# Optimization experiments

Hardware: AMD Instinct MI355X
Metric: run time of the kernel (lower is better)

Reference implementation:

```python
import jax, jax.numpy as jnp
import numpy as np
import math

D_MODEL = 2048
K = 64
W = 512              # window_size
STRIDE = W // 2      # = 256
EMA_ALPHA = 0.9
N_RETRIEVE = 8
EPS = 1e-12


def _build_cheby(k, w):
    # cheby_mat[k, n] = cos(k * arccos(t_n)), t_n = cos(pi*(2n+1)/(2w))
    ns = np.arange(w, dtype=np.float64)
    t = np.cos(np.pi * (2 * ns + 1) / (2 * w))
    ks = np.arange(k, dtype=np.float64)
    return jnp.asarray(np.cos(ks[:, None] * np.arccos(t)[None, :]), dtype=jnp.float32)


def setup_inputs() -> dict:
    key = jax.random.key(0)
    ks = jax.random.split(key, 5)
    B, S = 2, 8192
    scan_out = jax.random.normal(ks[0], (B, S, D_MODEL), dtype=jnp.float32)
    buf = jax.random.normal(ks[1], (W, D_MODEL), dtype=jnp.float32)  # pre-filled circular buffer
    # unit-modulus random-phase complex roles: r_k[d] = exp(i*theta)
    phases = jax.random.uniform(ks[2], (K, D_MODEL), dtype=jnp.float32) * (2.0 * math.pi)
    roles_real = jnp.cos(phases)
    roles_imag = jnp.sin(phases)
    w_bands = 1.0 / (jnp.arange(K, dtype=jnp.float32) + 1.0)  # w_init = 1/(k+1)
    retrieve_proj_w = jax.random.normal(ks[3], (D_MODEL, D_MODEL), dtype=jnp.float32) * 0.02
    inject_gate = jnp.zeros((1,), dtype=jnp.float32)
    cheby_mat = _build_cheby(K, W)
    return dict(scan_out=scan_out, buf=buf, roles_real=roles_real, roles_imag=roles_imag,
                w_bands=w_bands, retrieve_proj_w=retrieve_proj_w, inject_gate=inject_gate,
                cheby_mat=cheby_mat)


def reference(scan_out, buf, roles_real, roles_imag, w_bands, retrieve_proj_w, inject_gate, cheby_mat):
    S = scan_out.shape[1]
    h_mean = scan_out.mean(axis=0)                      # [S, D] batch-mean like torch code
    n_chunks = S // STRIDE
    chunks = h_mean.reshape(n_chunks, STRIDE, D_MODEL)  # each chunk triggers one bind

    init = (buf, jnp.int32(0),
            jnp.zeros((K, D_MODEL), jnp.float32),   # c_past
            jnp.zeros((D_MODEL,), jnp.float32),     # V_mem_real
            jnp.zeros((D_MODEL,), jnp.float32),     # V_mem_imag
            jnp.zeros((K,), jnp.float32),           # _coeff_norms (EMA)
            jnp.zeros((K,), jnp.float32))           # spectral_delta

    def step(carry, chunk):
        b, pos, c_past, vr, vi, cnorms, _ = carry
        # circular-buffer write of `stride` tokens starting at pos
        b = jax.lax.dynamic_update_slice(b, chunk, (pos, 0))
        pos = (pos + STRIDE) % W
        order = (jnp.arange(W, dtype=jnp.int32) + pos) % W   # oldest-first reorder
        data = b[order]                                      # [W, D]
        # Chebyshev coefficients: c = (2/W) * cheby_mat @ data, c0 halved
        coeffs = (2.0 / W) * (cheby_mat @ data)              # [K, D]
        coeffs = coeffs.at[0].multiply(0.5)
        # HRR-normalized bind into holographic memory via EMA
        norms = jnp.maximum(jnp.linalg.norm(coeffs, axis=-1, keepdims=True), EPS)
        cn = coeffs / norms
        cnorms = EMA_ALPHA * cnorms + (1.0 - EMA_ALPHA) * norms[:, 0]
        vr = EMA_ALPHA * vr + (1.0 - EMA_ALPHA) * (cn * roles_real).sum(axis=0)
        vi = EMA_ALPHA * vi + (1.0 - EMA_ALPHA) * (cn * roles_imag).sum(axis=0)
        # spectral delta vs previous window's coefficients
        delta = jnp.linalg.norm(coeffs - c_past, axis=-1)    # [K]
        return (b, pos, coeffs, vr, vi, cnorms, delta), None

    (b, pos, c_now, vr, vi, cnorms, delta), _ = jax.lax.scan(step, init, chunks)

    # retrieve: unbind top-J bands by spectral delta, denormalize, weight, project
    _, top = jax.lax.top_k(delta, N_RETRIEVE)                # [J]
    rr = roles_real[top]
    ri = roles_imag[top]
    retrieved = (vr[None, :] * rr + vi[None, :] * ri) * jnp.maximum(cnorms[top], EPS)[:, None]  # [J, D]
    weights = jax.nn.softplus(w_bands[top])                  # [J]
    ctx = (weights[:, None] * retrieved).sum(axis=0)         # [D]
    out = (ctx @ retrieve_proj_w.T) * jax.nn.sigmoid(inject_gate[0])  # [D]
    return out, delta, vr, vi
```

## Files before the change

### kernel.cpp

```cpp
#include <hip/hip_runtime.h>
#include <math.h>

#define D_MODEL 2048
#define KB_ 64
#define NCHUNK 32

typedef __bf16 bf16;
typedef __attribute__((ext_vector_type(8))) __bf16 bf16x8;
typedef __attribute__((ext_vector_type(4))) __bf16 bf16x4;
typedef __attribute__((ext_vector_type(4))) float f32x4;

#define OFF_PQ 0
#define N_PQ (33 * 128 * 2048)
#define OFF_NORMS N_PQ
#define OFF_PARTR (OFF_NORMS + 2048)
#define OFF_PARTI (OFF_PARTR + 32 * 2048)
#define OFF_CTX (OFF_PARTI + 32 * 2048)

__global__ __launch_bounds__(256, 4) void k1_mfma(
    const float* __restrict__ scan, const float* __restrict__ buf,
    const float* __restrict__ cheby, float* __restrict__ PQ)
{
  __shared__ bf16 As[128 * 72];
  __shared__ bf16 Bs[128 * 72];

  const int t = threadIdx.x;
  const int dtile = blockIdx.x, j = blockIdx.y;
  const int wid = t >> 6, lane = t & 63;
  const int wm = wid >> 1, wn = wid & 1;
  const int quad = lane >> 4, r16 = lane & 15;
  const int d0 = dtile * 128;
  const float* scan1 = scan + 8192 * 2048;

  f32x4 acc[4][4];
#pragma unroll
  for (int a = 0; a < 4; ++a)
#pragma unroll
    for (int b = 0; b < 4; ++b) acc[a][b] = (f32x4){0.f, 0.f, 0.f, 0.f};

  for (int nb = 0; nb < 4; ++nb) {
    __syncthreads();
#pragma unroll
    for (int i = 0; i < 8; ++i) {
      int flat = t + i * 256;
      int b = flat >> 4, q4 = flat & 15;
      const float* src = (b < 64) ? (cheby + b * 512 + nb * 64)
                                  : (cheby + (b - 64) * 512 + 256 + nb * 64);
      float4 v = *(const float4*)(src + q4 * 4);
      bf16x4 e = {(bf16)v.x, (bf16)v.y, (bf16)v.z, (bf16)v.w};
      *(bf16x4*)(As + b * 72 + q4 * 4) = e;
    }
#pragma unroll
    for (int i = 0; i < 8; ++i) {
      int p = t + i * 256;
      int d = p & 127;
      int n0 = (p >> 7) * 4;
      float v[4];
      if (j == 0) {
#pragma unroll
        for (int x = 0; x < 4; ++x)
          v[x] = buf[(256 + nb * 64 + n0 + x) * 2048 + d0 + d];
      } else {
        int base = ((j - 1) * 256 + nb * 64 + n0) * 2048 + d0 + d;
#pragma unroll
        for (int x = 0; x < 4; ++x)
          v[x] = 0.5f * (scan[base + x * 2048] + scan1[base + x * 2048]);
      }
      bf16x4 e = {(bf16)v[0], (bf16)v[1], (bf16)v[2], (bf16)v[3]};
      *(bf16x4*)(Bs + d * 72 + n0) = e;
    }
    __syncthreads();

#pragma unroll
    for (int ks = 0; ks < 2; ++ks) {
      bf16x8 af[4], bfr[4];
#pragma unroll
      for (int tm = 0; tm < 4; ++tm)
        af[tm] = *(const bf16x8*)(As + (wm * 64 + tm * 16 + r16) * 72 + ks * 32 + quad * 8);
#pragma unroll
      for (int tn = 0; tn < 4; ++tn)
        bfr[tn] = *(const bf16x8*)(Bs + (wn * 64 + tn * 16 + r16) * 72 + ks * 32 + quad * 8);
#pragma unroll
      for (int tm = 0; tm < 4; ++tm)
#pragma unroll
        for (int tn = 0; tn < 4; ++tn)
          acc[tm][tn] = __builtin_amdgcn_mfma_f32_16x16x32_bf16(
              af[tm], bfr[tn], acc[tm][tn], 0, 0, 0);
    }
  }

  const float scale = 2.0f / 512.0f;
#pragma unroll
  for (int tm = 0; tm < 4; ++tm) {
    int band_base = wm * 64 + tm * 16 + quad * 4;
#pragma unroll
    for (int tn = 0; tn < 4; ++tn) {
      int dc = d0 + wn * 64 + tn * 16 + r16;
#pragma unroll
      for (int r = 0; r < 4; ++r) {
        int band = band_base + r;
        float sc = (band == 0 || band == 64) ? scale * 0.5f : scale;
        PQ[(j * 128 + band) * 2048 + dc] = acc[tm][tn][r] * sc;
      }
    }
  }
}

__global__ __launch_bounds__(256) void k2_norms(
    const float* __restrict__ PQ, float* __restrict__ norms,
    float* __restrict__ dout)
{
  const int tid = threadIdx.x;
  const int b = blockIdx.x;
  float s = 0.f;
  if (b < NCHUNK * KB_) {
    int c = b >> 6, k = b & 63;
    const float* P = PQ + (c * 128 + k) * 2048;
    const float* Q = PQ + ((c + 1) * 128 + 64 + k) * 2048;
#pragma unroll
    for (int i = 0; i < 2; ++i) {
      float4 p = *(const float4*)(P + tid * 4 + i * 1024);
      float4 q = *(const float4*)(Q + tid * 4 + i * 1024);
      float x = p.x + q.x, y = p.y + q.y, z = p.z + q.z, w = p.w + q.w;
      s += x * x + y * y + z * z + w * w;
    }
  } else {
    int k = b - NCHUNK * KB_;
    const float* P1 = PQ + (31 * 128 + k) * 2048;
    const float* Q2 = PQ + (32 * 128 + 64 + k) * 2048;
    const float* P0 = PQ + (30 * 128 + k) * 2048;
    const float* Q1 = PQ + (31 * 128 + 64 + k) * 2048;
#pragma unroll
    for (int i = 0; i < 2; ++i) {
      float4 a = *(const float4*)(P1 + tid * 4 + i * 1024);
      float4 bb = *(const float4*)(Q2 + tid * 4 + i * 1024);
      float4 cc = *(const float4*)(P0 + tid * 4 + i * 1024);
      float4 dd = *(const float4*)(Q1 + tid * 4 + i * 1024);
      float x = a.x + bb.x - cc.x - dd.x, y = a.y + bb.y - cc.y - dd.y;
      float z = a.z + bb.z - cc.z - dd.z, w = a.w + bb.w - cc.w - dd.w;
      s += x * x + y * y + z * z + w * w;
    }
  }
  for (int o = 32; o > 0; o >>= 1) s += __shfl_down(s, o, 64);
  __shared__ float red[4];
  if ((tid & 63) == 0) red[tid >> 6] = s;
  __syncthreads();
  if (tid == 0) {
    float r = sqrtf(red[0] + red[1] + red[2] + red[3]);
    if (b < NCHUNK * KB_) norms[b] = fmaxf(r, 1e-12f);
    else dout[D_MODEL + (b - NCHUNK * KB_)] = r;
  }
}

__global__ __launch_bounds__(256) void k3_bind(
    const float* __restrict__ PQ, const float* __restrict__ norms,
    const float* __restrict__ rr, const float* __restrict__ ri,
    float* __restrict__ part_r, float* __restrict__ part_i)
{
  const int d4 = (blockIdx.x * 256 + threadIdx.x) * 4;
  const int c = blockIdx.y;
  const float wc = 0.1f * powf(0.9f, (float)(31 - c));
  float4 ar = make_float4(0.f, 0.f, 0.f, 0.f);
  float4 ai = make_float4(0.f, 0.f, 0.f, 0.f);
  for (int k = 0; k < KB_; ++k) {
    float4 p = *(const float4*)(PQ + (c * 128 + k) * 2048 + d4);
    float4 q = *(const float4*)(PQ + ((c + 1) * 128 + 64 + k) * 2048 + d4);
    float inv = 1.0f / norms[c * KB_ + k];
    float4 r = *(const float4*)(rr + k * D_MODEL + d4);
    float4 im = *(const float4*)(ri + k * D_MODEL + d4);
    float cx = (p.x + q.x) * inv, cy = (p.y + q.y) * inv;
    float cz = (p.z + q.z) * inv, cw = (p.w + q.w) * inv;
    ar.x += cx * r.x; ar.y += cy * r.y; ar.z += cz * r.z; ar.w += cw * r.w;
    ai.x += cx * im.x; ai.y += cy * im.y; ai.z += cz * im.z; ai.w += cw * im.w;
  }
  float4 outr = make_float4(wc * ar.x, wc * ar.y, wc * ar.z, wc * ar.w);
  float4 outi = make_float4(wc * ai.x, wc * ai.y, wc * ai.z, wc * ai.w);
  *(float4*)(part_r + c * D_MODEL + d4) = outr;
  *(float4*)(part_i + c * D_MODEL + d4) = outi;
}

__global__ __launch_bounds__(256) void k4_ctx(
    const float* __restrict__ norms, const float* __restrict__ part_r,
    const float* __restrict__ part_i, const float* __restrict__ rr,
    const float* __restrict__ ri, const float* __restrict__ wbands,
    float* __restrict__ dout, float* __restrict__ ctx)
{
  __shared__ float cn_s[64];
  __shared__ int top_s[8];
  __shared__ float wgt_s[8];
  const int tid = threadIdx.x;
  const int d = blockIdx.x * 256 + tid;
  if (tid < 64) {
    float s = 0.f;
    for (int c = 0; c < NCHUNK; ++c) s = 0.9f * s + 0.1f * norms[c * KB_ + tid];
    cn_s[tid] = fmaxf(s, 1e-12f);
  }
  __syncthreads();
  if (tid == 0) {
    unsigned long long taken = 0ULL;
    for (int jj = 0; jj < 8; ++jj) {
      float best = -1.f;
      int bi = 0;
      for (int k = 0; k < 64; ++k) {
        float dv = dout[D_MODEL + k];
        if (!((taken >> k) & 1ULL) && dv > best) { best = dv; bi = k; }
      }
      taken |= (1ULL << bi);
      top_s[jj] = bi;
      wgt_s[jj] = log1pf(expf(wbands[bi]));
    }
  }
  __syncthreads();
  float sr = 0.f, si = 0.f;
  for (int c = 0; c < NCHUNK; ++c) {
    sr += part_r[c * D_MODEL + d];
    si += part_i[c * D_MODEL + d];
  }
  dout[D_MODEL + KB_ + d] = sr;
  dout[D_MODEL + KB_ + D_MODEL + d] = si;
  float cx = 0.f;
#pragma unroll
  for (int jj = 0; jj < 8; ++jj) {
    int k = top_s[jj];
    cx += wgt_s[jj] * (sr * rr[k * D_MODEL + d] + si * ri[k * D_MODEL + d]) * cn_s[k];
  }
  ctx[d] = cx;
}

__global__ __launch_bounds__(256) void k5b_gemv(
    const float* __restrict__ Wp, const float* __restrict__ ctx,
    const float* __restrict__ gate, float* __restrict__ dout)
{
  const int tid = threadIdx.x;
  const int lane = tid & 63;
  const int w = tid >> 6;
  const int row = blockIdx.x * 4 + w;
  const float* p = Wp + row * D_MODEL;
  float s = 0.f;
#pragma unroll
  for (int i = 0; i < 8; ++i) {
    int e = lane * 4 + i * 256;
    float4 wv = *(const float4*)(p + e);
    float4 cv = *(const float4*)(ctx + e);
    s += wv.x * cv.x + wv.y * cv.y + wv.z * cv.z + wv.w * cv.w;
  }
  for (int o = 32; o > 0; o >>= 1) s += __shfl_down(s, o, 64);
  if (lane == 0) {
    float sig = 1.f / (1.f + expf(-gate[0]));
    dout[row] = s * sig;
  }
}

extern "C" void kernel_launch(void* const* d_in, const int* in_sizes, int n_in,
                              void* d_out, int out_size, void* d_ws, size_t ws_size,
                              hipStream_t stream) {
  const float* scan  = (const float*)d_in[0];
  const float* buf   = (const float*)d_in[1];
  const float* rr    = (const float*)d_in[2];
  const float* ri    = (const float*)d_in[3];
  const float* wb    = (const float*)d_in[4];
  const float* Wp    = (const float*)d_in[5];
  const float* gate  = (const float*)d_in[6];
  const float* cheby = (const float*)d_in[7];
  float* out = (float*)d_out;
  float* ws = (float*)d_ws;

  float* PQ     = ws + OFF_PQ;
  float* norms  = ws + OFF_NORMS;
  float* part_r = ws + OFF_PARTR;
  float* part_i = ws + OFF_PARTI;
  float* ctx    = ws + OFF_CTX;

  k1_mfma<<<dim3(16, 33), 256, 0, stream>>>(scan, buf, cheby, PQ);
  k2_norms<<<NCHUNK * KB_ + KB_, 256, 0, stream>>>(PQ, norms, out);
  k3_bind<<<dim3(2, NCHUNK), 256, 0, stream>>>(PQ, norms, rr, ri, part_r, part_i);
  k4_ctx<<<8, 256, 0, stream>>>(norms, part_r, part_i, rr, ri, wb, out, ctx);
  k5b_gemv<<<512, 256, 0, stream>>>(Wp, ctx, gate, out);
}
```

Baseline: 301.8 us.

## Compute full-window coefficients directly in MFMA kernel and fuse norm partials

Before, per-half-window partial coefficients (P/Q) were computed and summed in later kernels. Now each block handles one chunk's full 512-sample window against pre-converted bf16 Chebyshev rows and writes the final coefficients directly. The epilogue also emits per-tile squared-norm partials, which removes the separate norms kernel and the P+Q re-reads in the bind kernel. In exchange, overlapping scan rows are read twice, since adjacent windows share half their samples, and a small prep kernel and a delta kernel are added.

Result: faster. 279.6 us (-7.4%).

```diff
diff --git a/kernel.cpp b/kernel.cpp
--- a/kernel.cpp
+++ b/kernel.cpp
@@ -10,173 +10,165 @@
 typedef __attribute__((ext_vector_type(4))) __bf16 bf16x4;
 typedef __attribute__((ext_vector_type(4))) float f32x4;
 
-#define OFF_PQ 0
-#define N_PQ (33 * 128 * 2048)
-#define OFF_NORMS N_PQ
-#define OFF_PARTR (OFF_NORMS + 2048)
-#define OFF_PARTI (OFF_PARTR + 32 * 2048)
-#define OFF_CTX (OFF_PARTI + 32 * 2048)
-
-__global__ __launch_bounds__(256, 4) void k1_mfma(
+#define OFF_COEFFS 0
+#define OFF_NSQ    (32 * 64 * 2048)
+#define OFF_NORMS  (OFF_NSQ + 32 * 64 * 32)
+#define OFF_PARTR  (OFF_NORMS + 2048)
+#define OFF_PARTI  (OFF_PARTR + 32 * 2048)
+#define OFF_CTX    (OFF_PARTI + 32 * 2048)
+#define OFF_CHEB2  (OFF_CTX + 2048)
+
+__global__ __launch_bounds__(256) void k0_prep(
+    const float* __restrict__ cheby, bf16* __restrict__ cheb2)
+{
+  int flat = blockIdx.x * 256 + threadIdx.x;
+  cheb2[flat] = (bf16)cheby[flat];
+}
+
+__global__ __launch_bounds__(256) void k1_mfma(
     const float* __restrict__ scan, const float* __restrict__ buf,
-    const float* __restrict__ cheby, float* __restrict__ PQ)
-{
-  __shared__ bf16 As[128 * 72];
-  __shared__ bf16 Bs[128 * 72];
+    const bf16* __restrict__ cheb2, float* __restrict__ coeffs,
+    float* __restrict__ nsq_part)
+{
+  __shared__ bf16 Bs[64 * 72];
 
   const int t = threadIdx.x;
-  const int dtile = blockIdx.x, j = blockIdx.y;
-  const int wid = t >> 6, lane = t & 63;
-  const int wm = wid >> 1, wn = wid & 1;
+  const int dt = blockIdx.x;
+  const int c  = blockIdx.y;
+  const int w = t >> 6, lane = t & 63;
   const int quad = lane >> 4, r16 = lane & 15;
-  const int d0 = dtile * 128;
+  const int d0 = dt * 64;
+  const int n0 = (t >> 4) * 4;
+  const int d4 = (t & 15) * 4;
   const float* scan1 = scan + 8192 * 2048;
 
-  f32x4 acc[4][4];
-#pragma unroll
-  for (int a = 0; a < 4; ++a)
-#pragma unroll
-    for (int b = 0; b < 4; ++b) acc[a][b] = (f32x4){0.f, 0.f, 0.f, 0.f};
-
-  for (int nb = 0; nb < 4; ++nb) {
+  f32x4 acc[4];
+#pragma unroll
+  for (int tn = 0; tn < 4; ++tn) acc[tn] = (f32x4){0.f, 0.f, 0.f, 0.f};
+
+  for (int nb = 0; nb < 8; ++nb) {
+    const bf16* abase = cheb2 + (w * 16 + r16) * 512 + nb * 64 + quad * 8;
+    bf16x8 a0 = *(const bf16x8*)(abase);
+    bf16x8 a1 = *(const bf16x8*)(abase + 32);
+
+    float vv[4][4];
+    if (c == 0 && nb < 4) {
+      const float* bp = buf + (256 + nb * 64 + n0) * 2048 + d0 + d4;
+#pragma unroll
+      for (int i = 0; i < 4; ++i) {
+        float4 v = *(const float4*)(bp + i * 2048);
+        vv[i][0] = v.x; vv[i][1] = v.y; vv[i][2] = v.z; vv[i][3] = v.w;
+      }
+    } else {
+      int gbase = (c * 256 - 256 + nb * 64 + n0) * 2048 + d0 + d4;
+#pragma unroll
+      for (int i = 0; i < 4; ++i) {
+        float4 a = *(const float4*)(scan + gbase + i * 2048);
+        float4 b = *(const float4*)(scan1 + gbase + i * 2048);
+        vv[i][0] = 0.5f * (a.x + b.x); vv[i][1] = 0.5f * (a.y + b.y);
+        vv[i][2] = 0.5f * (a.z + b.z); vv[i][3] = 0.5f * (a.w + b.w);
+      }
+    }
     __syncthreads();
 #pragma unroll
-    for (int i = 0; i < 8; ++i) {
-      int flat = t + i * 256;
-      int b = flat >> 4, q4 = flat & 15;
-      const float* src = (b < 64) ? (cheby + b * 512 + nb * 64)
-                                  : (cheby + (b - 64) * 512 + 256 + nb * 64);
-      float4 v = *(const float4*)(src + q4 * 4);
-      bf16x4 e = {(bf16)v.x, (bf16)v.y, (bf16)v.z, (bf16)v.w};
-      *(bf16x4*)(As + b * 72 + q4 * 4) = e;
-    }
-#pragma unroll
-    for (int i = 0; i < 8; ++i) {
-      int p = t + i * 256;
-      int d = p & 127;
-      int n0 = (p >> 7) * 4;
-      float v[4];
-      if (j == 0) {
-#pragma unroll
-        for (int x = 0; x < 4; ++x)
-          v[x] = buf[(256 + nb * 64 + n0 + x) * 2048 + d0 + d];
-      } else {
-        int base = ((j - 1) * 256 + nb * 64 + n0) * 2048 + d0 + d;
-#pragma unroll
-        for (int x = 0; x < 4; ++x)
-          v[x] = 0.5f * (scan[base + x * 2048] + scan1[base + x * 2048]);
-      }
-      bf16x4 e = {(bf16)v[0], (bf16)v[1], (bf16)v[2], (bf16)v[3]};
-      *(bf16x4*)(Bs + d * 72 + n0) = e;
+    for (int x = 0; x < 4; ++x) {
+      bf16x4 e = {(bf16)vv[0][x], (bf16)vv[1][x], (bf16)vv[2][x], (bf16)vv[3][x]};
+      *(bf16x4*)(Bs + (d4 + x) * 72 + n0) = e;
     }
     __syncthreads();
 
 #pragma unroll
     for (int ks = 0; ks < 2; ++ks) {
-      bf16x8 af[4], bfr[4];
-#pragma unroll
-      for (int tm = 0; tm < 4; ++tm)
-        af[tm] = *(const bf16x8*)(As + (wm * 64 + tm * 16 + r16) * 72 + ks * 32 + quad * 8);
-#pragma unroll
-      for (int tn = 0; tn < 4; ++tn)
-        bfr[tn] = *(const bf16x8*)(Bs + (wn * 64 + tn * 16 + r16) * 72 + ks * 32 + quad * 8);
-#pragma unroll
-      for (int tm = 0; tm < 4; ++tm)
-#pragma unroll
-        for (int tn = 0; tn < 4; ++tn)
-          acc[tm][tn] = __builtin_amdgcn_mfma_f32_16x16x32_bf16(
-              af[tm], bfr[tn], acc[tm][tn], 0, 0, 0);
+      bf16x8 a = ks ? a1 : a0;
+#pragma unroll
+      for (int tn = 0; tn < 4; ++tn) {
+        bf16x8 bfr = *(const bf16x8*)(Bs + (tn * 16 + r16) * 72 + ks * 32 + quad * 8);
+        acc[tn] = __builtin_amdgcn_mfma_f32_16x16x32_bf16(a, bfr, acc[tn], 0, 0, 0);
+      }
     }
   }
 
   const float scale = 2.0f / 512.0f;
-#pragma unroll
-  for (int tm = 0; tm < 4; ++tm) {
-    int band_base = wm * 64 + tm * 16 + quad * 4;
-#pragma unroll
-    for (int tn = 0; tn < 4; ++tn) {
-      int dc = d0 + wn * 64 + tn * 16 + r16;
-#pragma unroll
-      for (int r = 0; r < 4; ++r) {
-        int band = band_base + r;
-        float sc = (band == 0 || band == 64) ? scale * 0.5f : scale;
-        PQ[(j * 128 + band) * 2048 + dc] = acc[tm][tn][r] * sc;
-      }
-    }
-  }
-}
-
-__global__ __launch_bounds__(256) void k2_norms(
-    const float* __restrict__ PQ, float* __restrict__ norms,
-    float* __restrict__ dout)
-{
-  const int tid = threadIdx.x;
-  const int b = blockIdx.x;
+  float sq[4] = {0.f, 0.f, 0.f, 0.f};
+#pragma unroll
+  for (int tn = 0; tn < 4; ++tn) {
+#pragma unroll
+    for (int rr = 0; rr < 4; ++rr) {
+      int band = w * 16 + quad * 4 + rr;
+      float sc = (band == 0) ? scale * 0.5f : scale;
+      float v = acc[tn][rr] * sc;
+      coeffs[(c * 64 + band) * 2048 + d0 + tn * 16 + r16] = v;
+      sq[rr] += v * v;
+    }
+  }
+#pragma unroll
+  for (int off = 8; off > 0; off >>= 1) {
+#pragma unroll
+    for (int rr = 0; rr < 4; ++rr) sq[rr] += __shfl_down(sq[rr], off);
+  }
+  if (r16 == 0) {
+#pragma unroll
+    for (int rr = 0; rr < 4; ++rr)
+      nsq_part[(c * 64 + w * 16 + quad * 4 + rr) * 32 + dt] = sq[rr];
+  }
+}
+
+__global__ __launch_bounds__(256) void kd_delta(
+    const float* __restrict__ coeffs, float* __restrict__ dout)
+{
+  const int k = blockIdx.x, tid = threadIdx.x;
+  const float* p1 = coeffs + (31 * 64 + k) * 2048;
+  const float* p0 = coeffs + (30 * 64 + k) * 2048;
   float s = 0.f;
-  if (b < NCHUNK * KB_) {
-    int c = b >> 6, k = b & 63;
-    const float* P = PQ + (c * 128 + k) * 2048;
-    const float* Q = PQ + ((c + 1) * 128 + 64 + k) * 2048;
-#pragma unroll
-    for (int i = 0; i < 2; ++i) {
-      float4 p = *(const float4*)(P + tid * 4 + i * 1024);
-      float4 q = *(const float4*)(Q + tid * 4 + i * 1024);
-      float x = p.x + q.x, y = p.y + q.y, z = p.z + q.z, w = p.w + q.w;
-      s += x * x + y * y + z * z + w * w;
-    }
-  } else {
-    int k = b - NCHUNK * KB_;
-    const float* P1 = PQ + (31 * 128 + k) * 2048;
-    const float* Q2 = PQ + (32 * 128 + 64 + k) * 2048;
-    const float* P0 = PQ + (30 * 128 + k) * 2048;
-    const float* Q1 = PQ + (31 * 128 + 64 + k) * 2048;
-#pragma unroll
-    for (int i = 0; i < 2; ++i) {
-      float4 a = *(const float4*)(P1 + tid * 4 + i * 1024);
-      float4 bb = *(const float4*)(Q2 + tid * 4 + i * 1024);
-      float4 cc = *(const float4*)(P0 + tid * 4 + i * 1024);
-      float4 dd = *(const float4*)(Q1 + tid * 4 + i * 1024);
-      float x = a.x + bb.x - cc.x - dd.x, y = a.y + bb.y - cc.y - dd.y;
-      float z = a.z + bb.z - cc.z - dd.z, w = a.w + bb.w - cc.w - dd.w;
-      s += x * x + y * y + z * z + w * w;
-    }
+#pragma unroll
+  for (int i = 0; i < 2; ++i) {
+    float4 a = *(const float4*)(p1 + tid * 4 + i * 1024);
+    float4 b = *(const float4*)(p0 + tid * 4 + i * 1024);
+    float x = a.x - b.x, y = a.y - b.y, z = a.z - b.z, ww = a.w - b.w;
+    s += x * x + y * y + z * z + ww * ww;
   }
   for (int o = 32; o > 0; o >>= 1) s += __shfl_down(s, o, 64);
   __shared__ float red[4];
   if ((tid & 63) == 0) red[tid >> 6] = s;
   __syncthreads();
-  if (tid == 0) {
-    float r = sqrtf(red[0] + red[1] + red[2] + red[3]);
-    if (b < NCHUNK * KB_) norms[b] = fmaxf(r, 1e-12f);
-    else dout[D_MODEL + (b - NCHUNK * KB_)] = r;
-  }
+  if (tid == 0) dout[D_MODEL + k] = sqrtf(red[0] + red[1] + red[2] + red[3]);
 }
 
 __global__ __launch_bounds__(256) void k3_bind(
-    const float* __restrict__ PQ, const float* __restrict__ norms,
+    const float* __restrict__ coeffs, const float* __restrict__ nsq_part,
     const float* __restrict__ rr, const float* __restrict__ ri,
-    float* __restrict__ part_r, float* __restrict__ part_i)
-{
-  const int d4 = (blockIdx.x * 256 + threadIdx.x) * 4;
+    float* __restrict__ part_r, float* __restrict__ part_i,
+    float* __restrict__ norms)
+{
+  __shared__ float inv_s[64];
+  const int tid = threadIdx.x;
   const int c = blockIdx.y;
+  if (tid < 64) {
+    float s = 0.f;
+#pragma unroll
+    for (int dt = 0; dt < 32; ++dt) s += nsq_part[(c * 64 + tid) * 32 + dt];
+    float nrm = fmaxf(sqrtf(s), 1e-12f);
+    inv_s[tid] = 1.0f / nrm;
+    if (blockIdx.x == 0) norms[c * 64 + tid] = nrm;
+  }
+  __syncthreads();
+  const int d4 = (blockIdx.x * 256 + tid) * 4;
   const float wc = 0.1f * powf(0.9f, (float)(31 - c));
   float4 ar = make_float4(0.f, 0.f, 0.f, 0.f);
   float4 ai = make_float4(0.f, 0.f, 0.f, 0.f);
   for (int k = 0; k < KB_; ++k) {
-    float4 p = *(const float4*)(PQ + (c * 128 + k) * 2048 + d4);
-    float4 q = *(const float4*)(PQ + ((c + 1) * 128 + 64 + k) * 2048 + d4);
-    float inv = 1.0f / norms[c * KB_ + k];
+    float4 cf = *(const float4*)(coeffs + (c * 64 + k) * 2048 + d4);
+    float inv = inv_s[k];
     float4 r = *(const float4*)(rr + k * D_MODEL + d4);
     float4 im = *(const float4*)(ri + k * D_MODEL + d4);
-    float cx = (p.x + q.x) * inv, cy = (p.y + q.y) * inv;
-    float cz = (p.z + q.z) * inv, cw = (p.w + q.w) * inv;
+    float cx = cf.x * inv, cy = cf.y * inv, cz = cf.z * inv, cw = cf.w * inv;
     ar.x += cx * r.x; ar.y += cy * r.y; ar.z += cz * r.z; ar.w += cw * r.w;
     ai.x += cx * im.x; ai.y += cy * im.y; ai.z += cz * im.z; ai.w += cw * im.w;
   }
-  float4 outr = make_float4(wc * ar.x, wc * ar.y, wc * ar.z, wc * ar.w);
-  float4 outi = make_float4(wc * ai.x, wc * ai.y, wc * ai.z, wc * ai.w);
-  *(float4*)(part_r + c * D_MODEL + d4) = outr;
-  *(float4*)(part_i + c * D_MODEL + d4) = outi;
+  *(float4*)(part_r + c * D_MODEL + d4) =
+      make_float4(wc * ar.x, wc * ar.y, wc * ar.z, wc * ar.w);
+  *(float4*)(part_i + c * D_MODEL + d4) =
+      make_float4(wc * ai.x, wc * ai.y, wc * ai.z, wc * ai.w);
 }
 
 __global__ __launch_bounds__(256) void k4_ctx(
@@ -192,7 +184,7 @@
   const int d = blockIdx.x * 256 + tid;
   if (tid < 64) {
     float s = 0.f;
-    for (int c = 0; c < NCHUNK; ++c) s = 0.9f * s + 0.1f * norms[c * KB_ + tid];
+    for (int c = 0; c < NCHUNK; ++c) s = 0.9f * s + 0.1f * norms[c * 64 + tid];
     cn_s[tid] = fmaxf(s, 1e-12f);
   }
   __syncthreads();
@@ -265,15 +257,19 @@
   float* out = (float*)d_out;
   float* ws = (float*)d_ws;
 
-  float* PQ     = ws + OFF_PQ;
-  float* norms  = ws + OFF_NORMS;
-  float* part_r = ws + OFF_PARTR;
-  float* part_i = ws + OFF_PARTI;
-  float* ctx    = ws + OFF_CTX;
-
-  k1_mfma<<<dim3(16, 33), 256, 0, stream>>>(scan, buf, cheby, PQ);
-  k2_norms<<<NCHUNK * KB_ + KB_, 256, 0, stream>>>(PQ, norms, out);
-  k3_bind<<<dim3(2, NCHUNK), 256, 0, stream>>>(PQ, norms, rr, ri, part_r, part_i);
+  float* coeffs   = ws + OFF_COEFFS;
+  float* nsq_part = ws + OFF_NSQ;
+  float* norms    = ws + OFF_NORMS;
+  float* part_r   = ws + OFF_PARTR;
+  float* part_i   = ws + OFF_PARTI;
+  float* ctx      = ws + OFF_CTX;
+  bf16*  cheb2    = (bf16*)(ws + OFF_CHEB2);
+
+  k0_prep<<<128, 256, 0, stream>>>(cheby, cheb2);
+  k1_mfma<<<dim3(32, 32), 256, 0, stream>>>(scan, buf, cheb2, coeffs, nsq_part);
+  kd_delta<<<64, 256, 0, stream>>>(coeffs, out);
+  k3_bind<<<dim3(2, NCHUNK), 256, 0, stream>>>(coeffs, nsq_part, rr, ri,
+                                               part_r, part_i, norms);
   k4_ctx<<<8, 256, 0, stream>>>(norms, part_r, part_i, rr, ri, wb, out, ctx);
   k5b_gemv<<<512, 256, 0, stream>>>(Wp, ctx, gate, out);
 }
```
